# Kernel optimization log

Measured on AMD Instinct MI355X. Metric: run time of the kernel, lower is better.

## Reference

```python
import jax, jax.numpy as jnp
import numpy as np

N, E, D_IN, HID, OUT, H = 50000, 800000, 64, 128, 128, 8


def _lin(key, fan_in, fan_out, bias=True):
    k1, k2 = jax.random.split(key)
    W = jax.random.normal(k1, (fan_in, fan_out), jnp.float32) / np.sqrt(fan_in)
    if bias:
        b = jax.random.normal(k2, (fan_out,), jnp.float32) * 0.01
        return W, b
    return (W,)


def setup_inputs() -> dict:
    key = jax.random.key(0)
    ks = jax.random.split(key, 40)
    inp = {
        "x": jax.random.normal(ks[0], (N, D_IN), jnp.float32),
        "edge_index": jax.random.randint(ks[1], (2, E), 0, N, jnp.int64),
        "edge_attr": jax.random.normal(ks[2], (E, D_IN), jnp.float32),
    }
    dims = [(D_IN, HID), (HID, HID), (HID, OUT)]  # (in, heads*out_ch) per layer
    ki = 3
    for l, (di, do) in enumerate(dims):
        inp[f"Wq{l}"], inp[f"bq{l}"] = _lin(ks[ki], di, do); ki += 1
        inp[f"Wk{l}"], inp[f"bk{l}"] = _lin(ks[ki], di, do); ki += 1
        inp[f"Wv{l}"], inp[f"bv{l}"] = _lin(ks[ki], di, do); ki += 1
        (inp[f"We{l}"],) = _lin(ks[ki], D_IN, do, bias=False); ki += 1
        inp[f"Ws{l}"], inp[f"bs{l}"] = _lin(ks[ki], di, do); ki += 1
    for l in range(2):
        inp[f"g{l}"] = jnp.ones((HID,), jnp.float32)
        inp[f"be{l}"] = jnp.zeros((HID,), jnp.float32)
    return inp


def _transformer_conv(x, src, dst, edge_attr, Wq, bq, Wk, bk, Wv, bv, We, Ws, bs):
    n = x.shape[0]
    hc = Wq.shape[1]
    c = hc // H
    q = (x @ Wq + bq).reshape(n, H, c)
    k = (x @ Wk + bk).reshape(n, H, c)
    v = (x @ Wv + bv).reshape(n, H, c)
    e = (edge_attr @ We).reshape(-1, H, c)  # [E,H,c]
    ke = k[src] + e                          # edge-wise key + edge proj
    alpha = jnp.einsum("ehc,ehc->eh", q[dst], ke) / jnp.sqrt(jnp.float32(c))
    m = jax.ops.segment_max(alpha, dst, num_segments=n)
    m = jnp.where(jnp.isfinite(m), m, 0.0)
    p = jnp.exp(alpha - m[dst])
    s = jax.ops.segment_sum(p, dst, num_segments=n)
    a = p / (s[dst] + 1e-16)                 # segment softmax over in-edges
    msg = (v[src] + e) * a[..., None]
    out = jax.ops.segment_sum(msg, dst, num_segments=n).reshape(n, hc)
    return out + x @ Ws + bs                 # root/skip connection


def _bn(x, g, b):
    mu = jnp.mean(x, axis=0)
    var = jnp.mean(jnp.square(x - mu), axis=0)
    return g * (x - mu) * jax.lax.rsqrt(var + 1e-5) + b


def reference(x, edge_index, edge_attr,
              Wq0, bq0, Wk0, bk0, Wv0, bv0, We0, Ws0, bs0,
              Wq1, bq1, Wk1, bk1, Wv1, bv1, We1, Ws1, bs1,
              Wq2, bq2, Wk2, bk2, Wv2, bv2, We2, Ws2, bs2,
              g0, be0, g1, be1):
    src, dst = edge_index[0], edge_index[1]
    h = _transformer_conv(x, src, dst, edge_attr, Wq0, bq0, Wk0, bk0, Wv0, bv0, We0, Ws0, bs0)
    h = jax.nn.relu(_bn(h, g0, be0))
    h = _transformer_conv(h, src, dst, edge_attr, Wq1, bq1, Wk1, bk1, Wv1, bv1, We1, Ws1, bs1)
    h = jax.nn.relu(_bn(h, g1, be1))
    h = _transformer_conv(h, src, dst, edge_attr, Wq2, bq2, Wk2, bk2, Wv2, bv2, We2, Ws2, bs2)
    return h, edge_attr
```

## Files before the change

### kernel.cpp

```cpp
#include <hip/hip_runtime.h>
#include <hip/hip_bf16.h>

typedef __attribute__((ext_vector_type(8))) short short8;
typedef __attribute__((ext_vector_type(4))) float f32x4;
typedef unsigned short ushort_t;
typedef __attribute__((ext_vector_type(2))) unsigned short ushort2v;

static __device__ __forceinline__ ushort_t f2bf(float x) {
    __hip_bfloat16 h = __float2bfloat16(x);
    return *(ushort_t*)&h;
}
static __device__ __forceinline__ float bflo(unsigned int u) { return __uint_as_float(u << 16); }
static __device__ __forceinline__ float bfhi(unsigned int u) { return __uint_as_float(u & 0xffff0000u); }
static __device__ __forceinline__ float bfu(ushort_t u) { return __uint_as_float((unsigned int)u << 16); }


__global__ void hist_kernel(const int* __restrict__ dst, int E, int* __restrict__ hist) {
    int i = blockIdx.x * blockDim.x + threadIdx.x;
    if (i < E) atomicAdd(&hist[dst[i]], 1);
}

__global__ __launch_bounds__(1024) void scan_block_kernel(
    const int* __restrict__ hist, int n, int* __restrict__ row_ptr, int* __restrict__ bsums)
{
    __shared__ int lds[1024];
    int tid = threadIdx.x;
    int i = blockIdx.x * 1024 + tid;
    int vv = (i < n) ? hist[i] : 0;
    lds[tid] = vv;
    __syncthreads();
    for (int off = 1; off < 1024; off <<= 1) {
        int t = (tid >= off) ? lds[tid - off] : 0;
        __syncthreads();
        lds[tid] += t;
        __syncthreads();
    }
    if (i < n) row_ptr[i] = lds[tid] - vv;
    if (tid == 1023) bsums[blockIdx.x] = lds[1023];
}

__global__ void scan_tops_kernel(int* __restrict__ bsums, int nb) {
    if (threadIdx.x == 0 && blockIdx.x == 0) {
        int run = 0;
        for (int i = 0; i < nb; i++) { int t = bsums[i]; bsums[i] = run; run += t; }
    }
}

__global__ __launch_bounds__(256) void scan_add_kernel(
    const int* __restrict__ bsums, int n, int total,
    int* __restrict__ row_ptr, int* __restrict__ cursor)
{
    int i = blockIdx.x * blockDim.x + threadIdx.x;
    if (i < n) {
        int vv = row_ptr[i] + bsums[i >> 10];
        row_ptr[i] = vv;
        cursor[i] = vv;
    }
    if (i == 0) row_ptr[n] = total;
}

__global__ void scatter_kernel(const int* __restrict__ src, const int* __restrict__ dst, int E,
                               int* __restrict__ cursor, int* __restrict__ eid, int* __restrict__ srcs) {
    int i = blockIdx.x * blockDim.x + threadIdx.x;
    if (i < E) {
        int d = dst[i];
        int pos = atomicAdd(&cursor[d], 1);
        eid[pos] = i;
        srcs[pos] = src[i];
    }
}

__global__ __launch_bounds__(256) void permute_ea_kernel(
    const float* __restrict__ edge_attr, const int* __restrict__ eid, int E,
    ushort_t* __restrict__ ea)
{
    int idx = blockIdx.x * blockDim.x + threadIdx.x;
    if (idx >= E * 8) return;
    int j = idx >> 3, seg = idx & 7;
    int rsrc = eid[j];
    const float* s = edge_attr + (size_t)rsrc * 64 + seg * 8;
    float4 f0 = *(const float4*)s;
    float4 f1 = *(const float4*)(s + 4);
    short8 o;
    o[0] = f2bf(f0.x); o[1] = f2bf(f0.y); o[2] = f2bf(f0.z); o[3] = f2bf(f0.w);
    o[4] = f2bf(f1.x); o[5] = f2bf(f1.y); o[6] = f2bf(f1.z); o[7] = f2bf(f1.w);
    *(short8*)(ea + (size_t)j * 64 + seg * 8) = o;
}

__global__ __launch_bounds__(256) void pack_Wnode_kernel(
    const float* __restrict__ Wq, const float* __restrict__ Wk,
    const float* __restrict__ Wv, const float* __restrict__ Ws,
    int DI, ushort_t* __restrict__ dst)
{
    int NKF = DI >> 5;
    int total = DI * 512;
    int idx = blockIdx.x * blockDim.x + threadIdx.x;
    if (idx >= total) return;
    int j = idx & 7;
    int lane = (idx >> 3) & 63;
    int rest = idx >> 9;
    int kf = rest % NKF;
    int t = rest / NKF;
    int kdim = kf * 32 + (lane >> 4) * 8 + j;
    int ncol = t * 16 + (lane & 15);
    const float* W = (ncol < 128) ? Wq : (ncol < 256) ? Wk : (ncol < 384) ? Wv : Ws;
    dst[idx] = f2bf(W[kdim * 128 + (ncol & 127)]);
}

__global__ __launch_bounds__(256) void pack_bias_kernel(
    const float* __restrict__ bq, const float* __restrict__ bk,
    const float* __restrict__ bv, const float* __restrict__ bs,
    float* __restrict__ dst)
{
    int i = threadIdx.x + blockIdx.x * blockDim.x;
    if (i >= 512) return;
    const float* b = (i < 128) ? bq : (i < 256) ? bk : (i < 384) ? bv : bs;
    dst[i] = b[i & 127];
}

__global__ __launch_bounds__(256) void pack_We_kernel(
    const float* __restrict__ We0, const float* __restrict__ We1,
    const float* __restrict__ We2, ushort_t* __restrict__ Bpack)
{
    int idx = blockIdx.x * blockDim.x + threadIdx.x;
    if (idx >= 3 * 8192) return;
    int j = idx & 7;
    int lane = (idx >> 3) & 63;
    int kk = (idx >> 9) & 1;
    int t = (idx >> 10) & 7;
    int layer = idx >> 13;
    const float* We = (layer == 0) ? We0 : (layer == 1) ? We1 : We2;
    int kdim = kk * 32 + (lane >> 4) * 8 + j;
    int ncol = t * 16 + (lane & 15);
    Bpack[idx] = f2bf(We[kdim * 128 + ncol]);
}

template <int DI, bool BN>
__global__ __launch_bounds__(256) void node_gemm_mfma_kernel(
    const float* __restrict__ hin, int N,
    const ushort_t* __restrict__ Bpack, const float* __restrict__ biasc,
    const float* __restrict__ scale, const float* __restrict__ shift,
    float* __restrict__ qout, ushort_t* __restrict__ kout,
    ushort_t* __restrict__ vout, float* __restrict__ skipout)
{
    constexpr int NKF = DI / 32;
    __shared__ float ctile[64][132];
    int wave = threadIdx.x >> 6;
    int lane = threadIdx.x & 63;
    int tid = threadIdx.x;
    int base = blockIdx.x * 64;
    int m0 = base + wave * 16;

    int mrow = min(m0 + (lane & 15), N - 1);
    const float* arow = hin + (size_t)mrow * DI;
    int koff = (lane >> 4) * 8;

    short8 a[NKF];
#pragma unroll
    for (int kf = 0; kf < NKF; kf++) {
        float4 fa = *(const float4*)(arow + kf * 32 + koff);
        float4 fb = *(const float4*)(arow + kf * 32 + koff + 4);
        if constexpr (BN) {
            int c0 = kf * 32 + koff;
            float4 sa = *(const float4*)(scale + c0);
            float4 sb = *(const float4*)(scale + c0 + 4);
            float4 ha = *(const float4*)(shift + c0);
            float4 hb = *(const float4*)(shift + c0 + 4);
            fa.x = fmaxf(fa.x * sa.x + ha.x, 0.f);
            fa.y = fmaxf(fa.y * sa.y + ha.y, 0.f);
            fa.z = fmaxf(fa.z * sa.z + ha.z, 0.f);
            fa.w = fmaxf(fa.w * sa.w + ha.w, 0.f);
            fb.x = fmaxf(fb.x * sb.x + hb.x, 0.f);
            fb.y = fmaxf(fb.y * sb.y + hb.y, 0.f);
            fb.z = fmaxf(fb.z * sb.z + hb.z, 0.f);
            fb.w = fmaxf(fb.w * sb.w + hb.w, 0.f);
        }
        short8 t;
        t[0] = f2bf(fa.x); t[1] = f2bf(fa.y); t[2] = f2bf(fa.z); t[3] = f2bf(fa.w);
        t[4] = f2bf(fb.x); t[5] = f2bf(fb.y); t[6] = f2bf(fb.z); t[7] = f2bf(fb.w);
        a[kf] = t;
    }

    const short8* Bp = (const short8*)Bpack;
    f32x4 acc[32];
#pragma unroll
    for (int t = 0; t < 32; t++) acc[t] = (f32x4){0.f, 0.f, 0.f, 0.f};
#pragma unroll
    for (int t = 0; t < 32; t++) {
#pragma unroll
        for (int kf = 0; kf < NKF; kf++)
            acc[t] = __builtin_amdgcn_mfma_f32_16x16x32_bf16(a[kf], Bp[(t * NKF + kf) * 64 + lane], acc[t], 0, 0, 0);
    }

    int crow = (lane >> 4) * 4;
    int ccol = lane & 15;
#pragma unroll
    for (int osel = 0; osel < 4; osel++) {
#pragma unroll
        for (int t8 = 0; t8 < 8; t8++) {
            float bb = biasc[osel * 128 + t8 * 16 + ccol];
#pragma unroll
            for (int r = 0; r < 4; r++)
                ctile[wave * 16 + crow + r][t8 * 16 + ccol] = acc[osel * 8 + t8][r] + bb;
        }
        __syncthreads();
        if (osel == 0 || osel == 3) {
            float* out = (osel == 0) ? qout : skipout;
#pragma unroll
            for (int it = 0; it < 8; it++) {
                int idx4 = it * 256 + tid;
                int row = idx4 >> 5;
                int c4 = idx4 & 31;
                int gr = base + row;
                if (gr < N) {
                    float4 vv = *(const float4*)&ctile[row][c4 * 4];
                    *(float4*)(out + (size_t)gr * 128 + c4 * 4) = vv;
                }
            }
        } else {
            ushort_t* out = (osel == 1) ? kout : vout;
#pragma unroll
            for (int it = 0; it < 4; it++) {
                int idx8 = it * 256 + tid;
                int row = idx8 >> 4;
                int c8 = idx8 & 15;
                int gr = base + row;
                if (gr < N) {
                    const float* s = &ctile[row][c8 * 8];
                    short8 vv;
#pragma unroll
                    for (int jj = 0; jj < 8; jj++) vv[jj] = f2bf(s[jj]);
                    *(short8*)(out + (size_t)gr * 128 + c8 * 8) = vv;
                }
            }
        }
        __syncthreads();
    }
}

__global__ __launch_bounds__(512) void agg_fused_kernel(
    const int* __restrict__ row_ptr, const int* __restrict__ srcs,
    const float* __restrict__ q, const ushort_t* __restrict__ k,
    const ushort_t* __restrict__ v, const ushort_t* __restrict__ ea,
    const ushort_t* __restrict__ BpackWe,
    float* __restrict__ hout, int N)
{
    __shared__ ushort_t bsh[8192];
    __shared__ ushort_t elds[8][16][136];
    int tid = threadIdx.x;
    {
        const short8* s8 = (const short8*)BpackWe;
        short8* d8 = (short8*)bsh;
        d8[tid] = s8[tid];
        d8[512 + tid] = s8[512 + tid];
    }
    __syncthreads();

    int wave = tid >> 6, lane = tid & 63;
    int n = blockIdx.x * 8 + wave;
    if (n >= N) return;

    const float2* q2 = (const float2*)q;
    const unsigned int* k32 = (const unsigned int*)k;
    const unsigned int* v32 = (const unsigned int*)v;
    float2* h2 = (float2*)hout;
    const short8* bs8 = (const short8*)bsh;

    int ch = lane & 15, kg = lane >> 4;
    float2 qq = q2[(size_t)n * 64 + lane];
    float2 sk = h2[(size_t)n * 64 + lane];
    float acc0 = 0.f, acc1 = 0.f, sw = 0.f;
    int jb = row_ptr[n], je = row_ptr[n + 1];

    short8 a0 = {}, a1 = {};
    int sv = 0;
    if (jb < je) {
        int j0 = min(jb + ch, je - 1);
        sv = srcs[j0];
        const ushort_t* row0 = ea + (size_t)j0 * 64;
        a0 = *(const short8*)(row0 + kg * 8);
        a1 = *(const short8*)(row0 + 32 + kg * 8);
    }

    for (int c0 = jb; c0 < je; c0 += 16) {
#pragma unroll
        for (int t = 0; t < 8; t++) {
            f32x4 z = (f32x4){0.f, 0.f, 0.f, 0.f};
            z = __builtin_amdgcn_mfma_f32_16x16x32_bf16(a0, bs8[(t * 2 + 0) * 64 + lane], z, 0, 0, 0);
            z = __builtin_amdgcn_mfma_f32_16x16x32_bf16(a1, bs8[(t * 2 + 1) * 64 + lane], z, 0, 0, 0);
#pragma unroll
            for (int r = 0; r < 4; r++)
                elds[wave][kg * 4 + r][t * 16 + ch] = f2bf(z[r]);
        }

        int cn = c0 + 16;
        short8 na0 = a0, na1 = a1;
        int nsv = sv;
        if (cn < je) {
            int jn = min(cn + ch, je - 1);
            nsv = srcs[jn];
            const ushort_t* nrow = ea + (size_t)jn * 64;
            na0 = *(const short8*)(nrow + kg * 8);
            na1 = *(const short8*)(nrow + 32 + kg * 8);
        }

        asm volatile("" ::: "memory");

        int cnt = min(16, je - c0);
        int r = 0;
        for (; r + 8 <= cnt; r += 8) {
            int s[8];
            ushort2v ee[8];
            unsigned int ku[8], vu[8];
#pragma unroll
            for (int u = 0; u < 8; u++) s[u] = __shfl(sv, r + u);
#pragma unroll
            for (int u = 0; u < 8; u++) ee[u] = *(const ushort2v*)&elds[wave][r + u][2 * lane];
#pragma unroll
            for (int u = 0; u < 8; u++) ku[u] = k32[(size_t)s[u] * 64 + lane];
#pragma unroll
            for (int u = 0; u < 8; u++) vu[u] = v32[(size_t)s[u] * 64 + lane];
            float p[8];
#pragma unroll
            for (int u = 0; u < 8; u++)
                p[u] = qq.x * (bflo(ku[u]) + bfu(ee[u][0])) + qq.y * (bfhi(ku[u]) + bfu(ee[u][1]));
#pragma unroll
            for (int u = 0; u < 8; u++) {
                p[u] += __shfl_xor(p[u], 1);
                p[u] += __shfl_xor(p[u], 2);
                p[u] += __shfl_xor(p[u], 4);
            }
            float w[8];
#pragma unroll
            for (int u = 0; u < 8; u++) w[u] = __expf(fminf(p[u] * 0.25f, 60.0f));
#pragma unroll
            for (int u = 0; u < 8; u++) {
                acc0 += w[u] * (bflo(vu[u]) + bfu(ee[u][0]));
                acc1 += w[u] * (bfhi(vu[u]) + bfu(ee[u][1]));
                sw += w[u];
            }
        }
        for (; r + 4 <= cnt; r += 4) {
            int s[4];
            ushort2v ee[4];
            unsigned int ku[4], vu[4];
#pragma unroll
            for (int u = 0; u < 4; u++) s[u] = __shfl(sv, r + u);
#pragma unroll
            for (int u = 0; u < 4; u++) ee[u] = *(const ushort2v*)&elds[wave][r + u][2 * lane];
#pragma unroll
            for (int u = 0; u < 4; u++) ku[u] = k32[(size_t)s[u] * 64 + lane];
#pragma unroll
            for (int u = 0; u < 4; u++) vu[u] = v32[(size_t)s[u] * 64 + lane];
            float p[4];
#pragma unroll
            for (int u = 0; u < 4; u++)
                p[u] = qq.x * (bflo(ku[u]) + bfu(ee[u][0])) + qq.y * (bfhi(ku[u]) + bfu(ee[u][1]));
#pragma unroll
            for (int u = 0; u < 4; u++) {
                p[u] += __shfl_xor(p[u], 1);
                p[u] += __shfl_xor(p[u], 2);
                p[u] += __shfl_xor(p[u], 4);
            }
#pragma unroll
            for (int u = 0; u < 4; u++) {
                float w = __expf(fminf(p[u] * 0.25f, 60.0f));
                acc0 += w * (bflo(vu[u]) + bfu(ee[u][0]));
                acc1 += w * (bfhi(vu[u]) + bfu(ee[u][1]));
                sw += w;
            }
        }
        for (; r < cnt; ++r) {
            int s = __shfl(sv, r);
            ushort2v ee = *(const ushort2v*)&elds[wave][r][2 * lane];
            unsigned int ku = k32[(size_t)s * 64 + lane];
            unsigned int vu = v32[(size_t)s * 64 + lane];
            float e0 = bfu(ee[0]), e1 = bfu(ee[1]);
            float part = qq.x * (bflo(ku) + e0) + qq.y * (bfhi(ku) + e1);
            part += __shfl_xor(part, 1);
            part += __shfl_xor(part, 2);
            part += __shfl_xor(part, 4);
            float w = __expf(fminf(part * 0.25f, 60.0f));
            acc0 += w * (bflo(vu) + e0);
            acc1 += w * (bfhi(vu) + e1);
            sw += w;
        }
        a0 = na0; a1 = na1; sv = nsv;
    }
    float inv = 1.0f / (sw + 1e-16f);
    float2 o;
    o.x = acc0 * inv + sk.x;
    o.y = acc1 * inv + sk.y;
    h2[(size_t)n * 64 + lane] = o;
}

__global__ __launch_bounds__(128) void bn_stats_kernel(const float* __restrict__ h, int N,
                                                       float* __restrict__ sums) {
    int f = threadIdx.x;
    float s = 0.f, s2 = 0.f;
    for (int n = blockIdx.x; n < N; n += gridDim.x) {
        float x = h[(size_t)n * 128 + f];
        s += x;
        s2 += x * x;
    }
    atomicAdd(&sums[f], s);
    atomicAdd(&sums[128 + f], s2);
}

__global__ __launch_bounds__(128) void bn_finalize_kernel(
    const float* __restrict__ sums, const float* __restrict__ g,
    const float* __restrict__ be, int N,
    float* __restrict__ scale, float* __restrict__ shift)
{
    int f = threadIdx.x;
    float invN = 1.0f / (float)N;
    float mu = sums[f] * invN;
    float var = sums[128 + f] * invN - mu * mu;
    float sc = g[f] * rsqrtf(var + 1e-5f);
    scale[f] = sc;
    shift[f] = be[f] - mu * sc;
}

extern "C" void kernel_launch(void* const* d_in, const int* in_sizes, int n_in,
                              void* d_out, int out_size, void* d_ws, size_t ws_size,
                              hipStream_t stream)
{
    const float* x = (const float*)d_in[0];
    const int* edge_index = (const int*)d_in[1];
    const float* edge_attr = (const float*)d_in[2];
    int N = in_sizes[0] / 64;
    int E = in_sizes[1] / 2;
    const int* src = edge_index;
    const int* dst = edge_index + E;

    const float* W[3][9];
    for (int l = 0; l < 3; l++)
        for (int i = 0; i < 9; i++) W[l][i] = (const float*)d_in[3 + l * 9 + i];
    const float* g0 = (const float*)d_in[30];
    const float* be0 = (const float*)d_in[31];
    const float* g1 = (const float*)d_in[32];
    const float* be1 = (const float*)d_in[33];

    char* p = (char*)d_ws;
    auto alloc = [&](size_t bytes) -> char* {
        char* r = p;
        p += (bytes + 255) & ~(size_t)255;
        return r;
    };
    float* q = (float*)alloc((size_t)N * 128 * 4);
    ushort_t* k = (ushort_t*)alloc((size_t)N * 128 * 2);
    ushort_t* v = (ushort_t*)alloc((size_t)N * 128 * 2);
    float* B = (float*)alloc((size_t)N * 128 * 4);
    ushort_t* ea = (ushort_t*)alloc((size_t)E * 64 * 2);
    int* row_ptr = (int*)alloc((size_t)(N + 1) * 4);
    int* cursor = (int*)alloc((size_t)N * 4);
    int* histb = (int*)alloc((size_t)N * 4);
    int* eid = (int*)alloc((size_t)E * 4);
    int* srcs = (int*)alloc((size_t)E * 4);
    int* bsums = (int*)alloc(64 * 4);
    float* sums = (float*)alloc(512 * 4);
    float* bnp = (float*)alloc(512 * 4);
    ushort_t* BpackE = (ushort_t*)alloc((size_t)3 * 8192 * 2);
    ushort_t* BpackN = (ushort_t*)alloc((size_t)3 * 65536 * 2);
    float* biasc = (float*)alloc((size_t)3 * 512 * 4);

    int nb = (N + 1023) / 1024;

    hipMemsetAsync(histb, 0, (size_t)N * 4, stream);
    hipMemsetAsync(sums, 0, 512 * 4, stream);
    hist_kernel<<<(E + 255) / 256, 256, 0, stream>>>(dst, E, histb);
    scan_block_kernel<<<nb, 1024, 0, stream>>>(histb, N, row_ptr, bsums);
    scan_tops_kernel<<<1, 64, 0, stream>>>(bsums, nb);
    scan_add_kernel<<<(N + 255) / 256, 256, 0, stream>>>(bsums, N, E, row_ptr, cursor);
    scatter_kernel<<<(E + 255) / 256, 256, 0, stream>>>(src, dst, E, cursor, eid, srcs);
    permute_ea_kernel<<<(E * 8 + 255) / 256, 256, 0, stream>>>(edge_attr, eid, E, ea);

    pack_We_kernel<<<(3 * 8192 + 255) / 256, 256, 0, stream>>>(W[0][6], W[1][6], W[2][6], BpackE);
    for (int l = 0; l < 3; l++) {
        int DI = (l == 0) ? 64 : 128;
        pack_Wnode_kernel<<<(DI * 512 + 255) / 256, 256, 0, stream>>>(
            W[l][0], W[l][2], W[l][4], W[l][7], DI, BpackN + (size_t)l * 65536);
        pack_bias_kernel<<<2, 256, 0, stream>>>(W[l][1], W[l][3], W[l][5], W[l][8],
                                                biasc + (size_t)l * 512);
    }

    for (int l = 0; l < 3; l++) {
        float* skipbuf = (l == 2) ? (float*)d_out : B;
        if (l == 0)
            node_gemm_mfma_kernel<64, false><<<(N + 63) / 64, 256, 0, stream>>>(
                x, N, BpackN, biasc, nullptr, nullptr, q, k, v, skipbuf);
        else
            node_gemm_mfma_kernel<128, true><<<(N + 63) / 64, 256, 0, stream>>>(
                B, N, BpackN + (size_t)l * 65536, biasc + (size_t)l * 512,
                bnp + (size_t)(l - 1) * 256, bnp + (size_t)(l - 1) * 256 + 128,
                q, k, v, skipbuf);
        agg_fused_kernel<<<(N + 7) / 8, 512, 0, stream>>>(
            row_ptr, srcs, q, k, v, ea, BpackE + (size_t)l * 8192, skipbuf, N);
        if (l < 2) {
            bn_stats_kernel<<<256, 128, 0, stream>>>(skipbuf, N, sums + (size_t)l * 256);
            const float* gg = (l == 0) ? g0 : g1;
            const float* bb = (l == 0) ? be0 : be1;
            bn_finalize_kernel<<<1, 128, 0, stream>>>(
                sums + (size_t)l * 256, gg, bb, N,
                bnp + (size_t)l * 256, bnp + (size_t)l * 256 + 128);
        }
    }

    hipMemcpyAsync((float*)d_out + (size_t)N * 128, edge_attr, (size_t)E * 64 * 4,
                   hipMemcpyDeviceToDevice, stream);
}
```

Measured before the change: 794.6 us.

## Interleave K and V into one buffer and prefetch gathers before edge MFMA

K and V bf16 rows are interleaved into a single kv buffer, so each edge gather is one 8-byte load per lane instead of two 4-byte loads from separate arrays. The gathers for all 16 edges in a chunk are issued via readlane before the edge-projection MFMAs, so their latency overlaps that compute. The 8/4/1 tail loops are replaced by two fixed 8-edge blocks that mask out-of-range edges, and the head reductions use DPP and ds_swizzle instead of shfl_xor. The costs are more registers for the prefetched kv values and wasted work on padded edges in small chunks.

```diff
diff --git a/kernel.cpp b/kernel.cpp
--- a/kernel.cpp
+++ b/kernel.cpp
@@ -5,6 +5,8 @@
 typedef __attribute__((ext_vector_type(4))) float f32x4;
 typedef unsigned short ushort_t;
 typedef __attribute__((ext_vector_type(2))) unsigned short ushort2v;
+typedef __attribute__((ext_vector_type(2))) unsigned int uint2v;
+typedef __attribute__((ext_vector_type(4))) unsigned int uint4v;
 
 static __device__ __forceinline__ ushort_t f2bf(float x) {
     __hip_bfloat16 h = __float2bfloat16(x);
@@ -13,6 +15,16 @@
 static __device__ __forceinline__ float bflo(unsigned int u) { return __uint_as_float(u << 16); }
 static __device__ __forceinline__ float bfhi(unsigned int u) { return __uint_as_float(u & 0xffff0000u); }
 static __device__ __forceinline__ float bfu(ushort_t u) { return __uint_as_float((unsigned int)u << 16); }
+
+template <int CTRL>
+static __device__ __forceinline__ float dpp_xadd(float x) {
+    int y = __builtin_amdgcn_update_dpp(0, __float_as_int(x), CTRL, 0xF, 0xF, true);
+    return x + __int_as_float(y);
+}
+static __device__ __forceinline__ float swz4_add(float x) {
+    int y = __builtin_amdgcn_ds_swizzle(__float_as_int(x), 0x101F);
+    return x + __int_as_float(y);
+}
 
 
 __global__ void hist_kernel(const int* __restrict__ dst, int E, int* __restrict__ hist) {
@@ -140,11 +152,12 @@
     const float* __restrict__ hin, int N,
     const ushort_t* __restrict__ Bpack, const float* __restrict__ biasc,
     const float* __restrict__ scale, const float* __restrict__ shift,
-    float* __restrict__ qout, ushort_t* __restrict__ kout,
-    ushort_t* __restrict__ vout, float* __restrict__ skipout)
+    float* __restrict__ qout, unsigned int* __restrict__ kvout,
+    float* __restrict__ skipout)
 {
     constexpr int NKF = DI / 32;
     __shared__ float ctile[64][132];
+    __shared__ ushort_t ctileK[64][136];
     int wave = threadIdx.x >> 6;
     int lane = threadIdx.x & 63;
     int tid = threadIdx.x;
@@ -194,55 +207,118 @@
 
     int crow = (lane >> 4) * 4;
     int ccol = lane & 15;
-#pragma unroll
-    for (int osel = 0; osel < 4; osel++) {
-#pragma unroll
-        for (int t8 = 0; t8 < 8; t8++) {
-            float bb = biasc[osel * 128 + t8 * 16 + ccol];
-#pragma unroll
-            for (int r = 0; r < 4; r++)
-                ctile[wave * 16 + crow + r][t8 * 16 + ccol] = acc[osel * 8 + t8][r] + bb;
+
+#pragma unroll
+    for (int t8 = 0; t8 < 8; t8++) {
+        float bb = biasc[t8 * 16 + ccol];
+#pragma unroll
+        for (int r = 0; r < 4; r++)
+            ctile[wave * 16 + crow + r][t8 * 16 + ccol] = acc[t8][r] + bb;
+    }
+    __syncthreads();
+#pragma unroll
+    for (int it = 0; it < 8; it++) {
+        int idx4 = it * 256 + tid;
+        int row = idx4 >> 5;
+        int c4 = idx4 & 31;
+        int gr = base + row;
+        if (gr < N)
+            *(float4*)(qout + (size_t)gr * 128 + c4 * 4) = *(const float4*)&ctile[row][c4 * 4];
+    }
+    __syncthreads();
+
+#pragma unroll
+    for (int t8 = 0; t8 < 8; t8++) {
+        float bb = biasc[128 + t8 * 16 + ccol];
+#pragma unroll
+        for (int r = 0; r < 4; r++)
+            ctileK[wave * 16 + crow + r][t8 * 16 + ccol] = f2bf(acc[8 + t8][r] + bb);
+    }
+#pragma unroll
+    for (int t8 = 0; t8 < 8; t8++) {
+        float bb = biasc[256 + t8 * 16 + ccol];
+#pragma unroll
+        for (int r = 0; r < 4; r++)
+            ctile[wave * 16 + crow + r][t8 * 16 + ccol] = acc[16 + t8][r] + bb;
+    }
+    __syncthreads();
+#pragma unroll
+    for (int it = 0; it < 4; it++) {
+        int idx8 = it * 256 + tid;
+        int row = idx8 >> 4;
+        int c8 = idx8 & 15;
+        int gr = base + row;
+        if (gr < N) {
+            const float* vs = &ctile[row][c8 * 8];
+            uint4v o0, o1;
+#pragma unroll
+            for (int i = 0; i < 4; i++) {
+                ushort2v kp2 = *(const ushort2v*)&ctileK[row][c8 * 8 + 2 * i];
+                unsigned int kp = (unsigned int)kp2[0] | ((unsigned int)kp2[1] << 16);
+                unsigned int vp = (unsigned int)f2bf(vs[2 * i]) | ((unsigned int)f2bf(vs[2 * i + 1]) << 16);
+                if (i < 2) { o0[2 * i] = kp; o0[2 * i + 1] = vp; }
+                else       { o1[2 * (i - 2)] = kp; o1[2 * (i - 2) + 1] = vp; }
+            }
+            unsigned int* dp = kvout + (size_t)gr * 128 + c8 * 8;
+            *(uint4v*)dp = o0;
+            *(uint4v*)(dp + 4) = o1;
         }
-        __syncthreads();
-        if (osel == 0 || osel == 3) {
-            float* out = (osel == 0) ? qout : skipout;
-#pragma unroll
-            for (int it = 0; it < 8; it++) {
-                int idx4 = it * 256 + tid;
-                int row = idx4 >> 5;
-                int c4 = idx4 & 31;
-                int gr = base + row;
-                if (gr < N) {
-                    float4 vv = *(const float4*)&ctile[row][c4 * 4];
-                    *(float4*)(out + (size_t)gr * 128 + c4 * 4) = vv;
-                }
-            }
-        } else {
-            ushort_t* out = (osel == 1) ? kout : vout;
-#pragma unroll
-            for (int it = 0; it < 4; it++) {
-                int idx8 = it * 256 + tid;
-                int row = idx8 >> 4;
-                int c8 = idx8 & 15;
-                int gr = base + row;
-                if (gr < N) {
-                    const float* s = &ctile[row][c8 * 8];
-                    short8 vv;
-#pragma unroll
-                    for (int jj = 0; jj < 8; jj++) vv[jj] = f2bf(s[jj]);
-                    *(short8*)(out + (size_t)gr * 128 + c8 * 8) = vv;
-                }
-            }
-        }
-        __syncthreads();
-    }
-}
+    }
+    __syncthreads();
+
+#pragma unroll
+    for (int t8 = 0; t8 < 8; t8++) {
+        float bb = biasc[384 + t8 * 16 + ccol];
+#pragma unroll
+        for (int r = 0; r < 4; r++)
+            ctile[wave * 16 + crow + r][t8 * 16 + ccol] = acc[24 + t8][r] + bb;
+    }
+    __syncthreads();
+#pragma unroll
+    for (int it = 0; it < 8; it++) {
+        int idx4 = it * 256 + tid;
+        int row = idx4 >> 5;
+        int c4 = idx4 & 31;
+        int gr = base + row;
+        if (gr < N)
+            *(float4*)(skipout + (size_t)gr * 128 + c4 * 4) = *(const float4*)&ctile[row][c4 * 4];
+    }
+}
+
+#define PROCESS8(B)                                                              \
+    {                                                                            \
+        ushort2v eev[8];                                                         \
+        float p[8];                                                              \
+        _Pragma("unroll")                                                        \
+        for (int u = 0; u < 8; u++)                                              \
+            eev[u] = *(const ushort2v*)&elds[wave][(B) * 8 + u][2 * lane];       \
+        _Pragma("unroll")                                                        \
+        for (int u = 0; u < 8; u++) {                                            \
+            uint2v kvp = kvr[(B) * 8 + u];                                       \
+            p[u] = qq.x * (bflo(kvp[0]) + bfu(eev[u][0]))                        \
+                 + qq.y * (bfhi(kvp[0]) + bfu(eev[u][1]));                       \
+        }                                                                        \
+        _Pragma("unroll")                                                        \
+        for (int u = 0; u < 8; u++) {                                            \
+            p[u] = dpp_xadd<0xB1>(p[u]);                                         \
+            p[u] = dpp_xadd<0x4E>(p[u]);                                         \
+            p[u] = swz4_add(p[u]);                                               \
+        }                                                                        \
+        _Pragma("unroll")                                                        \
+        for (int u = 0; u < 8; u++) {                                            \
+            float wv = __expf(fminf(p[u] * 0.25f, 60.0f));                       \
+            if (c0 + (B) * 8 + u >= je) wv = 0.f;                                \
+            uint2v kvp = kvr[(B) * 8 + u];                                       \
+            acc0 += wv * (bflo(kvp[1]) + bfu(eev[u][0]));                        \
+            acc1 += wv * (bfhi(kvp[1]) + bfu(eev[u][1]));                        \
+            sw += wv;                                                            \
+        }                                                                        \
+    }
 
 __global__ __launch_bounds__(512) void agg_fused_kernel(
     const int* __restrict__ row_ptr, const int* __restrict__ srcs,
-    const float* __restrict__ q, const ushort_t* __restrict__ k,
-    const ushort_t* __restrict__ v, const ushort_t* __restrict__ ea,
-    const ushort_t* __restrict__ BpackWe,
+    const float* __restrict__ q, const unsigned int* __restrict__ kvbuf,
+    const ushort_t* __restrict__ ea, const ushort_t* __restrict__ BpackWe,
     float* __restrict__ hout, int N)
 {
     __shared__ ushort_t bsh[8192];
@@ -261,8 +337,6 @@
     if (n >= N) return;
 
     const float2* q2 = (const float2*)q;
-    const unsigned int* k32 = (const unsigned int*)k;
-    const unsigned int* v32 = (const unsigned int*)v;
     float2* h2 = (float2*)hout;
     const short8* bs8 = (const short8*)bsh;
 
@@ -283,6 +357,13 @@
     }
 
     for (int c0 = jb; c0 < je; c0 += 16) {
+        uint2v kvr[16];
+#pragma unroll
+        for (int u = 0; u < 16; u++) {
+            int su = __builtin_amdgcn_readlane(sv, u);
+            kvr[u] = *(const uint2v*)(kvbuf + (size_t)su * 128 + 2 * lane);
+        }
+
 #pragma unroll
         for (int t = 0; t < 8; t++) {
             f32x4 z = (f32x4){0.f, 0.f, 0.f, 0.f};
@@ -306,85 +387,9 @@
 
         asm volatile("" ::: "memory");
 
-        int cnt = min(16, je - c0);
-        int r = 0;
-        for (; r + 8 <= cnt; r += 8) {
-            int s[8];
-            ushort2v ee[8];
-            unsigned int ku[8], vu[8];
-#pragma unroll
-            for (int u = 0; u < 8; u++) s[u] = __shfl(sv, r + u);
-#pragma unroll
-            for (int u = 0; u < 8; u++) ee[u] = *(const ushort2v*)&elds[wave][r + u][2 * lane];
-#pragma unroll
-            for (int u = 0; u < 8; u++) ku[u] = k32[(size_t)s[u] * 64 + lane];
-#pragma unroll
-            for (int u = 0; u < 8; u++) vu[u] = v32[(size_t)s[u] * 64 + lane];
-            float p[8];
-#pragma unroll
-            for (int u = 0; u < 8; u++)
-                p[u] = qq.x * (bflo(ku[u]) + bfu(ee[u][0])) + qq.y * (bfhi(ku[u]) + bfu(ee[u][1]));
-#pragma unroll
-            for (int u = 0; u < 8; u++) {
-                p[u] += __shfl_xor(p[u], 1);
-                p[u] += __shfl_xor(p[u], 2);
-                p[u] += __shfl_xor(p[u], 4);
-            }
-            float w[8];
-#pragma unroll
-            for (int u = 0; u < 8; u++) w[u] = __expf(fminf(p[u] * 0.25f, 60.0f));
-#pragma unroll
-            for (int u = 0; u < 8; u++) {
-                acc0 += w[u] * (bflo(vu[u]) + bfu(ee[u][0]));
-                acc1 += w[u] * (bfhi(vu[u]) + bfu(ee[u][1]));
-                sw += w[u];
-            }
-        }
-        for (; r + 4 <= cnt; r += 4) {
-            int s[4];
-            ushort2v ee[4];
-            unsigned int ku[4], vu[4];
-#pragma unroll
-            for (int u = 0; u < 4; u++) s[u] = __shfl(sv, r + u);
-#pragma unroll
-            for (int u = 0; u < 4; u++) ee[u] = *(const ushort2v*)&elds[wave][r + u][2 * lane];
-#pragma unroll
-            for (int u = 0; u < 4; u++) ku[u] = k32[(size_t)s[u] * 64 + lane];
-#pragma unroll
-            for (int u = 0; u < 4; u++) vu[u] = v32[(size_t)s[u] * 64 + lane];
-            float p[4];
-#pragma unroll
-            for (int u = 0; u < 4; u++)
-                p[u] = qq.x * (bflo(ku[u]) + bfu(ee[u][0])) + qq.y * (bfhi(ku[u]) + bfu(ee[u][1]));
-#pragma unroll
-            for (int u = 0; u < 4; u++) {
-                p[u] += __shfl_xor(p[u], 1);
-                p[u] += __shfl_xor(p[u], 2);
-                p[u] += __shfl_xor(p[u], 4);
-            }
-#pragma unroll
-            for (int u = 0; u < 4; u++) {
-                float w = __expf(fminf(p[u] * 0.25f, 60.0f));
-                acc0 += w * (bflo(vu[u]) + bfu(ee[u][0]));
-                acc1 += w * (bfhi(vu[u]) + bfu(ee[u][1]));
-                sw += w;
-            }
-        }
-        for (; r < cnt; ++r) {
-            int s = __shfl(sv, r);
-            ushort2v ee = *(const ushort2v*)&elds[wave][r][2 * lane];
-            unsigned int ku = k32[(size_t)s * 64 + lane];
-            unsigned int vu = v32[(size_t)s * 64 + lane];
-            float e0 = bfu(ee[0]), e1 = bfu(ee[1]);
-            float part = qq.x * (bflo(ku) + e0) + qq.y * (bfhi(ku) + e1);
-            part += __shfl_xor(part, 1);
-            part += __shfl_xor(part, 2);
-            part += __shfl_xor(part, 4);
-            float w = __expf(fminf(part * 0.25f, 60.0f));
-            acc0 += w * (bflo(vu) + e0);
-            acc1 += w * (bfhi(vu) + e1);
-            sw += w;
-        }
+        PROCESS8(0)
+        if (c0 + 8 < je) PROCESS8(1)
+
         a0 = na0; a1 = na1; sv = nsv;
     }
     float inv = 1.0f / (sw + 1e-16f);
@@ -448,8 +453,7 @@
         return r;
     };
     float* q = (float*)alloc((size_t)N * 128 * 4);
-    ushort_t* k = (ushort_t*)alloc((size_t)N * 128 * 2);
-    ushort_t* v = (ushort_t*)alloc((size_t)N * 128 * 2);
+    unsigned int* kvbuf = (unsigned int*)alloc((size_t)N * 512);
     float* B = (float*)alloc((size_t)N * 128 * 4);
     ushort_t* ea = (ushort_t*)alloc((size_t)E * 64 * 2);
     int* row_ptr = (int*)alloc((size_t)(N + 1) * 4);
@@ -488,14 +492,14 @@
         float* skipbuf = (l == 2) ? (float*)d_out : B;
         if (l == 0)
             node_gemm_mfma_kernel<64, false><<<(N + 63) / 64, 256, 0, stream>>>(
-                x, N, BpackN, biasc, nullptr, nullptr, q, k, v, skipbuf);
+                x, N, BpackN, biasc, nullptr, nullptr, q, kvbuf, skipbuf);
         else
             node_gemm_mfma_kernel<128, true><<<(N + 63) / 64, 256, 0, stream>>>(
                 B, N, BpackN + (size_t)l * 65536, biasc + (size_t)l * 512,
                 bnp + (size_t)(l - 1) * 256, bnp + (size_t)(l - 1) * 256 + 128,
-                q, k, v, skipbuf);
+                q, kvbuf, skipbuf);
         agg_fused_kernel<<<(N + 7) / 8, 512, 0, stream>>>(
-            row_ptr, srcs, q, k, v, ea, BpackE + (size_t)l * 8192, skipbuf, N);
+            row_ptr, srcs, q, kvbuf, ea, BpackE + (size_t)l * 8192, skipbuf, N);
         if (l < 2) {
             bn_stats_kernel<<<256, 128, 0, stream>>>(skipbuf, N, sums + (size_t)l * 256);
             const float* gg = (l == 0) ? g0 : g1;
```

Result: faster. 749.8 us (-5.6%).
